# Kernel optimization log

Hardware: AMD Instinct MI355X
Metric: run time of the kernel (lower is better)

## Reference

```python
import jax, jax.numpy as jnp
import numpy as np

B, H, S, D = 2, 16, 2048, 64

def setup_inputs() -> dict:
    key = jax.random.key(0)
    kq, kk, kv = jax.random.split(key, 3)
    Q = jax.random.normal(kq, (B, H, S, D), dtype=jnp.float32)
    K = jax.random.normal(kk, (B, H, S, D), dtype=jnp.float32)
    V = jax.random.normal(kv, (B, H, S, D), dtype=jnp.float32)
    return {"Q": Q, "K": K, "V": V}

def reference(Q, K, V):
    scale = 1.0 / jnp.sqrt(jnp.asarray(Q.shape[-1], dtype=Q.dtype))
    # [B,H,S,S] scores, scaled post-matmul to match torch source
    scores = jnp.einsum('bhqd,bhkd->bhqk', Q, K) * scale
    attn = jax.nn.softmax(scores, axis=-1)
    return jnp.einsum('bhqk,bhkd->bhqd', attn, V)
```

## Files before the change

kernel.cpp:

```cpp
#include <hip/hip_runtime.h>

typedef __bf16 bf16;
typedef __bf16 bf16x4 __attribute__((ext_vector_type(4)));
typedef __bf16 bf16x8 __attribute__((ext_vector_type(8)));
typedef float  f32x4  __attribute__((ext_vector_type(4)));

#define S_LEN 2048
#define DHEAD 64
#define BH    32
#define QB    64
#define KB    64
#define NT    (S_LEN / KB)

static __device__ __forceinline__ void async_cp16(const bf16* g, bf16* l) {
  __builtin_amdgcn_global_load_lds(
      (const __attribute__((address_space(1))) void*)g,
      (__attribute__((address_space(3))) void*)l, 16, 0, 0);
}

static __device__ __forceinline__ f32x4 mfma_bf16(bf16x8 a, bf16x8 b, f32x4 c) {
  return __builtin_amdgcn_mfma_f32_16x16x32_bf16(a, b, c, 0, 0, 0);
}

__global__ __launch_bounds__(256)
void kv_prep2(const float* __restrict__ K, const float* __restrict__ V,
              bf16* __restrict__ Kb, bf16* __restrict__ Vf) {
  __shared__ bf16 t[64][72];
  const int bh = blockIdx.x >> 5;
  const int kt = blockIdx.x & 31;
  const int tid = threadIdx.x;
  const size_t tbase = ((size_t)bh * S_LEN + kt * 64) * DHEAD;

  const float* ksrc = K + tbase;
  bf16* kdst = Kb + tbase;
#pragma unroll
  for (int it = 0; it < 2; ++it) {
    const int i = tid + it * 256;
    const float4 a = ((const float4*)ksrc)[2 * i];
    const float4 b = ((const float4*)ksrc)[2 * i + 1];
    bf16x8 o;
    o[0] = (bf16)a.x; o[1] = (bf16)a.y; o[2] = (bf16)a.z; o[3] = (bf16)a.w;
    o[4] = (bf16)b.x; o[5] = (bf16)b.y; o[6] = (bf16)b.z; o[7] = (bf16)b.w;
    ((bf16x8*)kdst)[i] = o;
  }

  const float* vsrc = V + tbase;
#pragma unroll
  for (int it = 0; it < 4; ++it) {
    const int i = tid + it * 256;
    const int r = i >> 4, c4 = (i & 15) << 2;
    const float4 v = *(const float4*)(vsrc + (size_t)r * DHEAD + c4);
    bf16x4 o;
    o[0] = (bf16)v.x; o[1] = (bf16)v.y; o[2] = (bf16)v.z; o[3] = (bf16)v.w;
    *(bf16x4*)&t[r][c4] = o;
  }
  __syncthreads();

  bf16* vdst = Vf + (size_t)bh * S_LEN * DHEAD + (size_t)kt * 4096;
  const int lane = tid & 63, nd = tid >> 6;
  const int lg = lane >> 4, l15 = lane & 15;
#pragma unroll
  for (int h = 0; h < 2; ++h) {
    bf16x8 o;
#pragma unroll
    for (int j = 0; j < 8; ++j)
      o[j] = t[32 * h + 16 * (j >> 2) + 4 * lg + (j & 3)][nd * 16 + l15];
    *(bf16x8*)(vdst + ((nd * 2 + h) * 64 + lane) * 8) = o;
  }
}

__global__ __launch_bounds__(256, 4)
void attn_fwd7(const float* __restrict__ Qg0, const bf16* __restrict__ Kb0,
               const bf16* __restrict__ Vf0, float* __restrict__ Og0) {
  __shared__ __align__(16) bf16 Kl[2][KB * DHEAD];

  const int tid = threadIdx.x, wid = tid >> 6, lane = tid & 63;
  const int l15 = lane & 15, lg = lane >> 4;
  const int bid = blockIdx.x;
  const int swz = ((bid & 7) << 7) | (bid >> 3);
  const int bh = swz >> 5;
  const int qb = swz & 31;
  const int qbase = qb * QB + wid * 16;

  const float* Qg = Qg0 + (size_t)bh * S_LEN * DHEAD;
  const bf16* Kb = Kb0 + (size_t)bh * S_LEN * DHEAD;
  const bf16* Vf = Vf0 + (size_t)bh * S_LEN * DHEAD;
  float* Og = Og0 + (size_t)bh * S_LEN * DHEAD;

  const int srow = wid * 8 + (lane >> 3);
  const int scl = ((lane & 7) ^ (srow & 7)) << 3;
  const bf16* kg0 = Kb + (size_t)srow * DHEAD + scl;

#define STAGE(b, t)                                            \
  do {                                                         \
    const bf16* kg_ = kg0 + (size_t)(t) * KB * DHEAD;          \
    async_cp16(kg_, &Kl[b][wid * 512]);                        \
    async_cp16(kg_ + 32 * DHEAD, &Kl[b][2048 + wid * 512]);    \
  } while (0)

  const float qscale = 0.125f * 1.44269504088896341f;
  bf16x8 qfrag[2];
  {
    const float* qrow = Qg + (size_t)(qbase + l15) * DHEAD;
#pragma unroll
    for (int h = 0; h < 2; ++h) {
      const float* p = qrow + h * 32 + lg * 8;
      const float4 a = *(const float4*)(p);
      const float4 b = *(const float4*)(p + 4);
      bf16x8 f;
      f[0] = (bf16)(a.x * qscale); f[1] = (bf16)(a.y * qscale);
      f[2] = (bf16)(a.z * qscale); f[3] = (bf16)(a.w * qscale);
      f[4] = (bf16)(b.x * qscale); f[5] = (bf16)(b.y * qscale);
      f[6] = (bf16)(b.z * qscale); f[7] = (bf16)(b.w * qscale);
      qfrag[h] = f;
    }
  }

  float m_l = -__builtin_inff();
  float l_l = 0.f;
  f32x4 o_acc[4];
#pragma unroll
  for (int nd = 0; nd < 4; ++nd) o_acc[nd] = f32x4{0.f, 0.f, 0.f, 0.f};

  const int kxor = (l15 & 7) << 4;
  const bf16* vlane = Vf + lane * 8;

  STAGE(0, 0);
  __syncthreads();

  for (int kt = 0; kt < NT; ++kt) {
    const int cur = kt & 1;
    if (kt + 1 < NT) STAGE(cur ^ 1, kt + 1);

    bf16x8 vf[2][4];
    {
      const bf16* vb = vlane + (size_t)kt * 4096;
#pragma unroll
      for (int nd = 0; nd < 4; ++nd)
#pragma unroll
        for (int h = 0; h < 2; ++h)
          vf[h][nd] = *(const bf16x8*)(vb + (nd * 2 + h) * 512);
    }

    f32x4 sacc[4] = {};
    __builtin_amdgcn_s_setprio(1);
#pragma unroll
    for (int ns = 0; ns < 4; ++ns) {
      const int krow = ns * 16 + l15;
#pragma unroll
      for (int h = 0; h < 2; ++h) {
        const int kb = krow * 128 + ((((h << 2) + lg) << 4) ^ kxor);
        const bf16x8 kf = *(const bf16x8*)((const char*)&Kl[cur][0] + kb);
        sacc[ns] = mfma_bf16(kf, qfrag[h], sacc[ns]);
      }
    }
    __builtin_amdgcn_s_setprio(0);

    float pmax = sacc[0][0];
#pragma unroll
    for (int ns = 0; ns < 4; ++ns)
#pragma unroll
      for (int r = 0; r < 4; ++r) pmax = fmaxf(pmax, sacc[ns][r]);

    if (!__all(pmax <= m_l + 8.f)) {
      pmax = fmaxf(pmax, __shfl_xor(pmax, 16));
      pmax = fmaxf(pmax, __shfl_xor(pmax, 32));
      const float mn = fmaxf(m_l, pmax);
      const float alpha = __builtin_amdgcn_exp2f(m_l - mn);
      m_l = mn;
      l_l *= alpha;
#pragma unroll
      for (int r = 0; r < 4; ++r) {
        const float a_r = __shfl(alpha, (lane & 48) | (((lane >> 4) & 3) * 4 + r));
        o_acc[0][r] *= a_r;
        o_acc[1][r] *= a_r;
        o_acc[2][r] *= a_r;
        o_acc[3][r] *= a_r;
      }
    }

    float rsum = 0.f;
#pragma unroll
    for (int ns = 0; ns < 4; ++ns)
#pragma unroll
      for (int r = 0; r < 4; ++r) {
        const float p = __builtin_amdgcn_exp2f(sacc[ns][r] - m_l);
        sacc[ns][r] = p;
        rsum += p;
      }
    l_l += rsum;

    bf16x8 pa[2];
#pragma unroll
    for (int r = 0; r < 4; ++r) {
      pa[0][r]     = (bf16)sacc[0][r];
      pa[0][r + 4] = (bf16)sacc[1][r];
      pa[1][r]     = (bf16)sacc[2][r];
      pa[1][r + 4] = (bf16)sacc[3][r];
    }

    __builtin_amdgcn_s_setprio(1);
#pragma unroll
    for (int h = 0; h < 2; ++h)
#pragma unroll
      for (int nd = 0; nd < 4; ++nd)
        o_acc[nd] = mfma_bf16(pa[h], vf[h][nd], o_acc[nd]);
    __builtin_amdgcn_s_setprio(0);
    __syncthreads();
  }

  l_l += __shfl_xor(l_l, 16);
  l_l += __shfl_xor(l_l, 32);
#pragma unroll
  for (int r = 0; r < 4; ++r) {
    const float l_r = __shfl(l_l, (lane & 48) | (((lane >> 4) & 3) * 4 + r));
    const float inv = 1.0f / l_r;
    float* orow = Og + (size_t)(qbase + lg * 4 + r) * DHEAD;
#pragma unroll
    for (int nd = 0; nd < 4; ++nd)
      orow[nd * 16 + l15] = o_acc[nd][r] * inv;
  }
#undef STAGE
}

__global__ __launch_bounds__(256, 2)
void attn_fb(const float* __restrict__ Qg0, const float* __restrict__ Kg0,
             const float* __restrict__ Vg0, float* __restrict__ Og0) {
  __shared__ __align__(16) bf16 Kl[KB][72];
  __shared__ __align__(16) bf16 Vt[DHEAD][72];
  __shared__ __align__(16) bf16 Pl[4][16][72];
  const int tid = threadIdx.x, wid = tid >> 6, lane = tid & 63;
  const int l15 = lane & 15, lg = lane >> 4;
  const int bh = blockIdx.x >> 5, qb = blockIdx.x & 31;
  const int qbase = qb * 64 + wid * 16;
  const size_t base = (size_t)bh * S_LEN * DHEAD;
  const float* Qg = Qg0 + base;
  const float* Kg = Kg0 + base;
  const float* Vg = Vg0 + base;
  float* Og = Og0 + base;
  const float qscale = 0.125f * 1.44269504088896341f;
  bf16x8 qfrag[2];
  {
    const float* qrow = Qg + (size_t)(qbase + l15) * DHEAD;
#pragma unroll
    for (int h = 0; h < 2; ++h) {
      const float* p = qrow + h * 32 + lg * 8;
      const float4 a = *(const float4*)(p);
      const float4 b = *(const float4*)(p + 4);
      bf16x8 f;
      f[0] = (bf16)(a.x * qscale); f[1] = (bf16)(a.y * qscale);
      f[2] = (bf16)(a.z * qscale); f[3] = (bf16)(a.w * qscale);
      f[4] = (bf16)(b.x * qscale); f[5] = (bf16)(b.y * qscale);
      f[6] = (bf16)(b.z * qscale); f[7] = (bf16)(b.w * qscale);
      qfrag[h] = f;
    }
  }
  float m_r[4], l_r[4];
  f32x4 o_acc[4];
#pragma unroll
  for (int r = 0; r < 4; ++r) {
    m_r[r] = -__builtin_inff();
    l_r[r] = 0.f;
    o_acc[r] = f32x4{0.f, 0.f, 0.f, 0.f};
  }
  for (int kt = 0; kt < NT; ++kt) {
    __syncthreads();
#pragma unroll
    for (int it = 0; it < 4; ++it) {
      const int i = tid + it * 256;
      const int row = i >> 4, c4 = (i & 15) << 2;
      const float4 kk = *(const float4*)(Kg + (size_t)(kt * KB + row) * DHEAD + c4);
      bf16x4 kb;
      kb[0] = (bf16)kk.x; kb[1] = (bf16)kk.y; kb[2] = (bf16)kk.z; kb[3] = (bf16)kk.w;
      *(bf16x4*)&Kl[row][c4] = kb;
      const float4 vv = *(const float4*)(Vg + (size_t)(kt * KB + row) * DHEAD + c4);
      Vt[c4 + 0][row] = (bf16)vv.x;
      Vt[c4 + 1][row] = (bf16)vv.y;
      Vt[c4 + 2][row] = (bf16)vv.z;
      Vt[c4 + 3][row] = (bf16)vv.w;
    }
    __syncthreads();
    f32x4 sacc[4] = {};
#pragma unroll
    for (int ns = 0; ns < 4; ++ns)
#pragma unroll
      for (int h = 0; h < 2; ++h) {
        const bf16x8 kf = *(const bf16x8*)&Kl[ns * 16 + l15][h * 32 + lg * 8];
        sacc[ns] = mfma_bf16(qfrag[h], kf, sacc[ns]);
      }
    float rmax[4], alpha[4], rsum[4];
#pragma unroll
    for (int r = 0; r < 4; ++r)
      rmax[r] = fmaxf(fmaxf(sacc[0][r], sacc[1][r]), fmaxf(sacc[2][r], sacc[3][r]));
#pragma unroll
    for (int off = 1; off < 16; off <<= 1)
#pragma unroll
      for (int r = 0; r < 4; ++r)
        rmax[r] = fmaxf(rmax[r], __shfl_xor(rmax[r], off));
#pragma unroll
    for (int r = 0; r < 4; ++r) {
      const float mn = fmaxf(m_r[r], rmax[r]);
      alpha[r] = exp2f(m_r[r] - mn);
      m_r[r] = mn;
      rsum[r] = 0.f;
    }
#pragma unroll
    for (int ns = 0; ns < 4; ++ns)
#pragma unroll
      for (int r = 0; r < 4; ++r) {
        const float p = exp2f(sacc[ns][r] - m_r[r]);
        sacc[ns][r] = p;
        rsum[r] += p;
      }
#pragma unroll
    for (int off = 1; off < 16; off <<= 1)
#pragma unroll
      for (int r = 0; r < 4; ++r)
        rsum[r] += __shfl_xor(rsum[r], off);
#pragma unroll
    for (int r = 0; r < 4; ++r) {
      l_r[r] = l_r[r] * alpha[r] + rsum[r];
      o_acc[0][r] *= alpha[r];
      o_acc[1][r] *= alpha[r];
      o_acc[2][r] *= alpha[r];
      o_acc[3][r] *= alpha[r];
    }
#pragma unroll
    for (int ns = 0; ns < 4; ++ns)
#pragma unroll
      for (int r = 0; r < 4; ++r)
        Pl[wid][lg * 4 + r][ns * 16 + l15] = (bf16)sacc[ns][r];
    asm volatile("s_waitcnt lgkmcnt(0)" ::: "memory");
#pragma unroll
    for (int h = 0; h < 2; ++h) {
      const bf16x8 pf = *(const bf16x8*)&Pl[wid][l15][h * 32 + lg * 8];
#pragma unroll
      for (int nd = 0; nd < 4; ++nd) {
        const bf16x8 vf = *(const bf16x8*)&Vt[nd * 16 + l15][h * 32 + lg * 8];
        o_acc[nd] = mfma_bf16(pf, vf, o_acc[nd]);
      }
    }
  }
#pragma unroll
  for (int r = 0; r < 4; ++r) {
    const float inv = 1.0f / l_r[r];
    float* orow = Og + (size_t)(qbase + lg * 4 + r) * DHEAD;
#pragma unroll
    for (int nd = 0; nd < 4; ++nd)
      orow[nd * 16 + l15] = o_acc[nd][r] * inv;
  }
}

extern "C" void kernel_launch(void* const* d_in, const int* in_sizes, int n_in,
                              void* d_out, int out_size, void* d_ws, size_t ws_size,
                              hipStream_t stream) {
  const float* Q = (const float*)d_in[0];
  const float* K = (const float*)d_in[1];
  const float* V = (const float*)d_in[2];
  float* O = (float*)d_out;

  const size_t elems = (size_t)BH * S_LEN * DHEAD;
  const size_t bf16_bytes = elems * 2;
  if (ws_size >= 2 * bf16_bytes) {
    bf16* Kb = (bf16*)d_ws;
    bf16* Vf = (bf16*)((char*)d_ws + bf16_bytes);
    hipLaunchKernelGGL(kv_prep2, dim3(BH * 32), dim3(256), 0, stream, K, V, Kb, Vf);
    hipLaunchKernelGGL(attn_fwd7, dim3(BH * (S_LEN / QB)), dim3(256), 0, stream,
                       Q, Kb, Vf, O);
  } else {
    hipLaunchKernelGGL(attn_fb, dim3(1024), dim3(256), 0, stream, Q, K, V, O);
  }
}
```

Measured before the change: 141.8 us.

## Software-pipeline QK^T of next tile with softmax and PV of current tile

Restructures the attention main loop so the QK^T MFMAs for tile t+1 are issued before the softmax and PV of tile t, ping-ponging two score accumulators. K staging now prefetches two tiles ahead, with a single barrier at the top of each iteration. The max and sum reductions become tree-shaped, and launch bounds drop from 4 to 3 waves per SIMD to leave room for the extra accumulator registers. The goal is to overlap MFMA work with exp/VALU work, at the cost of more VGPRs and possibly lower occupancy.

```diff
diff --git a/kernel.cpp b/kernel.cpp
--- a/kernel.cpp
+++ b/kernel.cpp
@@ -69,8 +69,8 @@
   }
 }
 
-__global__ __launch_bounds__(256, 4)
-void attn_fwd7(const float* __restrict__ Qg0, const bf16* __restrict__ Kb0,
+__global__ __launch_bounds__(256, 3)
+void attn_fwd8(const float* __restrict__ Qg0, const bf16* __restrict__ Kb0,
                const bf16* __restrict__ Vf0, float* __restrict__ Og0) {
   __shared__ __align__(16) bf16 Kl[2][KB * DHEAD];
 
@@ -125,16 +125,31 @@
   const int kxor = (l15 & 7) << 4;
   const bf16* vlane = Vf + lane * 8;
 
-  STAGE(0, 0);
-  __syncthreads();
-
-  for (int kt = 0; kt < NT; ++kt) {
-    const int cur = kt & 1;
-    if (kt + 1 < NT) STAGE(cur ^ 1, kt + 1);
+  f32x4 saccA[4], saccB[4];
+
+  auto qkt = [&](f32x4 (&SN)[4], int b) {
+    __builtin_amdgcn_s_setprio(1);
+#pragma unroll
+    for (int ns = 0; ns < 4; ++ns) {
+      SN[ns] = f32x4{0.f, 0.f, 0.f, 0.f};
+      const int krow = ns * 16 + l15;
+#pragma unroll
+      for (int h = 0; h < 2; ++h) {
+        const int kb = krow * 128 + ((((h << 2) + lg) << 4) ^ kxor);
+        const bf16x8 kf = *(const bf16x8*)((const char*)&Kl[b][0] + kb);
+        SN[ns] = mfma_bf16(kf, qfrag[h], SN[ns]);
+      }
+    }
+    __builtin_amdgcn_s_setprio(0);
+  };
+
+  auto iter = [&](f32x4 (&SC)[4], f32x4 (&SN)[4], int t) {
+    __syncthreads();
+    if (t + 2 < NT) STAGE(t & 1, t + 2);
 
     bf16x8 vf[2][4];
     {
-      const bf16* vb = vlane + (size_t)kt * 4096;
+      const bf16* vb = vlane + (size_t)t * 4096;
 #pragma unroll
       for (int nd = 0; nd < 4; ++nd)
 #pragma unroll
@@ -142,25 +157,13 @@
           vf[h][nd] = *(const bf16x8*)(vb + (nd * 2 + h) * 512);
     }
 
-    f32x4 sacc[4] = {};
-    __builtin_amdgcn_s_setprio(1);
-#pragma unroll
-    for (int ns = 0; ns < 4; ++ns) {
-      const int krow = ns * 16 + l15;
-#pragma unroll
-      for (int h = 0; h < 2; ++h) {
-        const int kb = krow * 128 + ((((h << 2) + lg) << 4) ^ kxor);
-        const bf16x8 kf = *(const bf16x8*)((const char*)&Kl[cur][0] + kb);
-        sacc[ns] = mfma_bf16(kf, qfrag[h], sacc[ns]);
-      }
-    }
-    __builtin_amdgcn_s_setprio(0);
-
-    float pmax = sacc[0][0];
-#pragma unroll
-    for (int ns = 0; ns < 4; ++ns)
-#pragma unroll
-      for (int r = 0; r < 4; ++r) pmax = fmaxf(pmax, sacc[ns][r]);
+    if (t + 1 < NT) qkt(SN, (t + 1) & 1);
+
+    float m01 = fmaxf(fmaxf(SC[0][0], SC[0][1]), fmaxf(SC[0][2], SC[0][3]));
+    float m23 = fmaxf(fmaxf(SC[1][0], SC[1][1]), fmaxf(SC[1][2], SC[1][3]));
+    float m45 = fmaxf(fmaxf(SC[2][0], SC[2][1]), fmaxf(SC[2][2], SC[2][3]));
+    float m67 = fmaxf(fmaxf(SC[3][0], SC[3][1]), fmaxf(SC[3][2], SC[3][3]));
+    float pmax = fmaxf(fmaxf(m01, m23), fmaxf(m45, m67));
 
     if (!__all(pmax <= m_l + 8.f)) {
       pmax = fmaxf(pmax, __shfl_xor(pmax, 16));
@@ -179,24 +182,25 @@
       }
     }
 
-    float rsum = 0.f;
+    float s[4][4];
 #pragma unroll
     for (int ns = 0; ns < 4; ++ns)
 #pragma unroll
-      for (int r = 0; r < 4; ++r) {
-        const float p = __builtin_amdgcn_exp2f(sacc[ns][r] - m_l);
-        sacc[ns][r] = p;
-        rsum += p;
-      }
+      for (int r = 0; r < 4; ++r)
+        s[ns][r] = __builtin_amdgcn_exp2f(SC[ns][r] - m_l);
+    float rsum = ((s[0][0] + s[0][1]) + (s[0][2] + s[0][3]))
+               + ((s[1][0] + s[1][1]) + (s[1][2] + s[1][3]))
+               + ((s[2][0] + s[2][1]) + (s[2][2] + s[2][3]))
+               + ((s[3][0] + s[3][1]) + (s[3][2] + s[3][3]));
     l_l += rsum;
 
     bf16x8 pa[2];
 #pragma unroll
     for (int r = 0; r < 4; ++r) {
-      pa[0][r]     = (bf16)sacc[0][r];
-      pa[0][r + 4] = (bf16)sacc[1][r];
-      pa[1][r]     = (bf16)sacc[2][r];
-      pa[1][r + 4] = (bf16)sacc[3][r];
+      pa[0][r]     = (bf16)s[0][r];
+      pa[0][r + 4] = (bf16)s[1][r];
+      pa[1][r]     = (bf16)s[2][r];
+      pa[1][r + 4] = (bf16)s[3][r];
     }
 
     __builtin_amdgcn_s_setprio(1);
@@ -206,7 +210,16 @@
       for (int nd = 0; nd < 4; ++nd)
         o_acc[nd] = mfma_bf16(pa[h], vf[h][nd], o_acc[nd]);
     __builtin_amdgcn_s_setprio(0);
-    __syncthreads();
+  };
+
+  STAGE(0, 0);
+  __syncthreads();
+  STAGE(1, 1);
+  qkt(saccA, 0);
+
+  for (int kt = 0; kt < NT; kt += 2) {
+    iter(saccA, saccB, kt);
+    iter(saccB, saccA, kt + 1);
   }
 
   l_l += __shfl_xor(l_l, 16);
@@ -365,7 +378,7 @@
     bf16* Kb = (bf16*)d_ws;
     bf16* Vf = (bf16*)((char*)d_ws + bf16_bytes);
     hipLaunchKernelGGL(kv_prep2, dim3(BH * 32), dim3(256), 0, stream, K, V, Kb, Vf);
-    hipLaunchKernelGGL(attn_fwd7, dim3(BH * (S_LEN / QB)), dim3(256), 0, stream,
+    hipLaunchKernelGGL(attn_fwd8, dim3(BH * (S_LEN / QB)), dim3(256), 0, stream,
                        Q, Kb, Vf, O);
   } else {
     hipLaunchKernelGGL(attn_fb, dim3(1024), dim3(256), 0, stream, Q, K, V, O);
```

After: 143.5 us. No clear change (+1.2%).
